# Kernel optimization log

Measured on AMD Instinct MI355X. Metric: run time of the kernel, lower is better.

## Reference

```python
import jax, jax.numpy as jnp
import numpy as np

N = 50000   # num nodes
D = 128     # dim_h = d_model = d_inner (expand=1)
E = 500000  # num edges
B, L = 4, 4096
K = 4       # d_conv
DS = 16     # d_state
DTR = 8     # dt_rank = ceil(128/16)


def setup_inputs() -> dict:
    key = jax.random.key(0)
    ks = jax.random.split(key, 32)
    rn = lambda i, shape, s=0.05: jax.random.normal(ks[i], shape, jnp.float32) * s
    inp = {}
    inp["graph_embeddings"] = jax.random.normal(ks[0], (N, D), jnp.float32)
    inp["graph_edges"] = jax.random.randint(ks[1], (2, E), 0, N)
    # unique node indices so the final scatter matches torch advanced indexing
    inp["sequence"] = jax.random.permutation(ks[2], N)[: B * L].reshape(B, L)
    # GatedGCN linears A,B,D,E (dim_h -> dim_h)
    inp["WA"] = rn(3, (D, D)); inp["bA"] = jnp.zeros((D,), jnp.float32)
    inp["WB"] = rn(4, (D, D)); inp["bB"] = jnp.zeros((D,), jnp.float32)
    inp["WD"] = rn(5, (D, D)); inp["bD"] = jnp.zeros((D,), jnp.float32)
    inp["WE"] = rn(6, (D, D)); inp["bE"] = jnp.zeros((D,), jnp.float32)
    # Mamba params
    inp["W_in"] = rn(7, (D, 2 * D))                 # in_proj (bias=False)
    inp["conv_w"] = rn(8, (D, 1, K))                # depthwise causal conv
    inp["conv_b"] = jnp.zeros((D,), jnp.float32)
    inp["W_x"] = rn(9, (D, DTR + 2 * DS))           # x_proj (bias=False)
    inp["W_dt"] = rn(10, (DTR, D))
    inp["b_dt"] = jnp.zeros((D,), jnp.float32)
    A_init = jnp.tile(jnp.arange(1, DS + 1, dtype=jnp.float32)[None, :], (D, 1))
    inp["A_log"] = jnp.log(A_init)
    inp["D_ssm"] = jnp.ones((D,), jnp.float32)
    inp["W_out"] = rn(11, (D, D))                   # out_proj (bias=False)
    # FFN
    inp["W1"] = rn(12, (D, 2 * D)); inp["b1"] = jnp.zeros((2 * D,), jnp.float32)
    inp["W2"] = rn(13, (2 * D, D)); inp["b2"] = jnp.zeros((D,), jnp.float32)
    return inp


def _gatedgcn(x, edges, WA, bA, WB, bB, WD, bD, WE, bE):
    src, dst = edges[0], edges[1]
    Ax = x @ WA + bA
    Bx = x @ WB + bB
    Dx = x @ WD + bD
    Ex = x @ WE + bE
    sigma = jax.nn.sigmoid(Dx[dst] + Ex[src])          # [E, D] edge gates
    num = jax.ops.segment_sum(sigma * Bx[src], dst, num_segments=N)
    den = jax.ops.segment_sum(sigma, dst, num_segments=N)
    out = Ax + num / (den + 1e-6)
    return x + jax.nn.relu(out)                        # residual (dropout=0, eval)


def _mamba(x, W_in, conv_w, conv_b, W_x, W_dt, b_dt, A_log, D_ssm, W_out):
    # x: [B, L, D]
    xz = x @ W_in
    xm, z = jnp.split(xz, 2, axis=-1)
    xc = jnp.transpose(xm, (0, 2, 1))                  # [B, D, L]
    xc = jax.lax.conv_general_dilated(
        xc, conv_w, (1,), [(K - 1, 0)],
        dimension_numbers=("NCH", "OIH", "NCH"), feature_group_count=D)
    xc = xc + conv_b[None, :, None]
    xm = jax.nn.silu(jnp.transpose(xc, (0, 2, 1)))     # [B, L, D]
    x_dbl = xm @ W_x
    dt, Bm, Cm = jnp.split(x_dbl, [DTR, DTR + DS], axis=-1)
    delta = jax.nn.softplus(dt @ W_dt + b_dt)          # [B, L, D]
    A = -jnp.exp(A_log)                                # [D, DS]
    dA = jnp.exp(delta[..., None] * A)                 # [B, L, D, DS]
    dBx = delta[..., None] * Bm[:, :, None, :] * xm[..., None]

    def step(h, t):
        dA_t, dBx_t, C_t = t
        h = dA_t * h + dBx_t                           # [B, D, DS]
        y = jnp.einsum("bdn,bn->bd", h, C_t)
        return h, y

    h0 = jnp.zeros((x.shape[0], D, DS), xm.dtype)
    _, ys = jax.lax.scan(step, h0, (jnp.swapaxes(dA, 0, 1),
                                    jnp.swapaxes(dBx, 0, 1),
                                    jnp.swapaxes(Cm, 0, 1)))
    y = jnp.swapaxes(ys, 0, 1) + xm * D_ssm
    y = y * jax.nn.silu(z)
    return y @ W_out


def reference(graph_embeddings, WA, bA, WB, bB, WD, bD, WE, bE,
              W_in, conv_w, conv_b, W_x, W_dt, b_dt, A_log, D_ssm, W_out,
              W1, b1, W2, b2, graph_edges, sequence):
    h_in1 = graph_embeddings[sequence]                 # [B, L, D]
    h_local = _gatedgcn(graph_embeddings, graph_edges, WA, bA, WB, bB, WD, bD, WE, bE)
    h1 = h_local[sequence]
    h_attn = h_in1 + _mamba(h_in1, W_in, conv_w, conv_b, W_x, W_dt, b_dt, A_log, D_ssm, W_out)
    h = h1 + h_attn
    h = h + (jax.nn.relu(h @ W1 + b1) @ W2 + b2)       # residual FFN
    flat = sequence.reshape(-1)
    emb = graph_embeddings.at[flat].set(
        0.5 * graph_embeddings[flat] + 0.5 * h.reshape(-1, D))
    return emb
```

## Files before the change

kernel.cpp:

```cpp
#include <hip/hip_runtime.h>
#include <hip/hip_bf16.h>

#define N_NODES 50000
#define DIM     128
#define NEDGE   500000
#define BB      4
#define LL      4096
#define NTOK    (BB*LL)
#define DSTATE  16
#define DTRANK  8
#define SCH     16
#define NCH     (LL/SCH)
#define NBDN    (BB*DIM*DSTATE)

typedef __attribute__((ext_vector_type(8))) short short8;
typedef __attribute__((ext_vector_type(4))) float f32x4;

static __device__ __forceinline__ float sigmoidf_(float x){ return 1.f/(1.f+__expf(-x)); }
static __device__ __forceinline__ float siluf_(float x){ return x/(1.f+__expf(-x)); }
static __device__ __forceinline__ float softplusf_(float x){ return (x > 20.f) ? x : log1pf(__expf(x)); }
static __device__ __forceinline__ short f2bf(float f){
  union { float f; unsigned u; } v; v.f = f;
  unsigned r = v.u + 0x7FFFu + ((v.u >> 16) & 1u);
  return (short)(r >> 16);
}
static __device__ __forceinline__ unsigned cvt2bf(float a, float b){
  unsigned r;
  asm("v_cvt_pk_bf16_f32 %0, %1, %2" : "=v"(r) : "v"(a), "v"(b));
  return r;
}
static __device__ __forceinline__ float bf2f(unsigned short u){
  union { unsigned u; float f; } v; v.u = ((unsigned)u) << 16; return v.f;
}

__global__ void prep_k(const float* __restrict__ x, const int* __restrict__ seq,
                       const float* __restrict__ WA, const float* __restrict__ WB,
                       const float* __restrict__ WD, const float* __restrict__ WE,
                       const float* __restrict__ W_in, const float* __restrict__ Wout,
                       const float* __restrict__ W1, const float* __restrict__ W2,
                       const float* __restrict__ W_x,
                       short* __restrict__ wpak, short* __restrict__ xbf,
                       short* __restrict__ hseqbf, int* __restrict__ invmap,
                       int* __restrict__ cnt){
  int blk = blockIdx.x, tid = threadIdx.x;
  if (blk < 736){
    int i = blk*256 + tid;
    float v;
    if (i < 32768){ int n=i>>7, k=i&127; v = (n<128)? WB[k*128+n] : WE[k*128+n-128]; }
    else if (i < 65536){ int j=i-32768, n=j>>7, k=j&127; v = (n<128)? WA[k*128+n] : WD[k*128+n-128]; }
    else if (i < 98304){ int j=i-65536, n=j>>7, k=j&127; v = W_in[k*256+n]; }
    else if (i < 131072){ int j=i-98304, n=j>>7, k=j&127; v = W1[k*256+n]; }
    else if (i < 163840){ int j=i-131072, n=j>>8, k=j&255; v = W2[k*128+n]; }
    else if (i < 180224){ int j=i-163840, n=j>>7, k=j&127; v = Wout[k*128+n]; }
    else if (i < 188416){ int j=i-180224, n=j>>7, k=j&127; v = (n<40)? W_x[k*40+n] : 0.f; }
    else return;
    wpak[i] = f2bf(v);
  } else if (blk < 3861){
    int i = (blk-736)*256 + tid;
    const float4 v0 = *(const float4*)(x + (size_t)i*8);
    const float4 v1 = *(const float4*)(x + (size_t)i*8 + 4);
    union { int4 q; short8 s; } w;
    w.q.x = cvt2bf(v0.x, v0.y); w.q.y = cvt2bf(v0.z, v0.w);
    w.q.z = cvt2bf(v1.x, v1.y); w.q.w = cvt2bf(v1.z, v1.w);
    *(short8*)(xbf + (size_t)i*8) = w.s;
  } else if (blk < 4885){
    int i = (blk-3861)*256 + tid;
    int t = i >> 4, cc = i & 15;
    const float* src = x + (size_t)seq[t]*128 + cc*8;
    const float4 v0 = *(const float4*)src;
    const float4 v1 = *(const float4*)(src + 4);
    union { int4 q; short8 s; } w;
    w.q.x = cvt2bf(v0.x, v0.y); w.q.y = cvt2bf(v0.z, v0.w);
    w.q.z = cvt2bf(v1.x, v1.y); w.q.w = cvt2bf(v1.z, v1.w);
    *(short8*)(hseqbf + (size_t)t*128 + cc*8) = w.s;
  } else if (blk < 4949){
    int i = (blk-4885)*256 + tid;
    if (i < NTOK) invmap[seq[i]] = i;
  } else {
    int i = (blk-4949)*256 + tid;
    if (i < 16384) cnt[i] = 0;
  }
}

template<int NCG, int KF, int EPI>
__global__ __launch_bounds__(256) void gemm4_k(const short* __restrict__ A,
    const short* __restrict__ Wt, const float* __restrict__ bias,
    float* __restrict__ C, short* __restrict__ C16, int ldc, int nsteps){
  const int K = KF*32;
  const int tid = threadIdx.x;
  const int wave = tid >> 6, lane = tid & 63;
  const int lr = lane & 15, kg = lane >> 4;
  const int cg = wave % NCG, rg = wave / NCG;
  const int RPB = 16*(4/NCG);

  short8 wf[4][KF];
  #pragma unroll
  for (int f=0; f<4; ++f){
    const short* wp = Wt + (size_t)(cg*64 + f*16 + lr)*K + kg*8;
    #pragma unroll
    for (int ks=0; ks<KF; ++ks) wf[f][ks] = *(const short8*)(wp + ks*32);
  }
  float4 bfv[4];
  #pragma unroll
  for (int f=0; f<4; ++f)
    bfv[f] = bias ? *(const float4*)&bias[cg*64 + f*16 + kg*4] : make_float4(0,0,0,0);

  int step = blockIdx.x;
  short8 a0[KF], a1[KF];
  if (step < nsteps){
    const short* p = A + ((size_t)step*RPB + rg*16 + lr)*K + kg*8;
    #pragma unroll
    for (int ks=0; ks<KF; ++ks) a0[ks] = *(const short8*)(p + ks*32);
  }
  for (; step < nsteps; step += gridDim.x){
    int nstep = step + gridDim.x;
    if (nstep < nsteps){
      const short* p = A + ((size_t)nstep*RPB + rg*16 + lr)*K + kg*8;
      #pragma unroll
      for (int ks=0; ks<KF; ++ks) a1[ks] = *(const short8*)(p + ks*32);
    }
    f32x4 acc[4];
    #pragma unroll
    for (int f=0; f<4; ++f) acc[f] = (f32x4){0.f,0.f,0.f,0.f};
    #pragma unroll
    for (int f=0; f<4; ++f)
      #pragma unroll
      for (int ks=0; ks<KF; ++ks)
        acc[f] = __builtin_amdgcn_mfma_f32_16x16x32_bf16(wf[f][ks], a0[ks], acc[f], 0,0,0);

    int row = step*RPB + rg*16 + lr;
    #pragma unroll
    for (int f=0; f<4; ++f){
      int col = cg*64 + f*16 + kg*4;
      size_t idx = (size_t)row*ldc + col;
      float v0 = acc[f][0]+bfv[f].x, v1 = acc[f][1]+bfv[f].y;
      float v2 = acc[f][2]+bfv[f].z, v3 = acc[f][3]+bfv[f].w;
      if (EPI == 0){
        *(float4*)&C[idx] = make_float4(v0,v1,v2,v3);
      } else if (EPI == 2){
        float4 c = *(const float4*)&C[idx];
        *(float4*)&C[idx] = make_float4(c.x+v0, c.y+v1, c.z+v2, c.w+v3);
      } else if (EPI == 3){
        uint2 u; u.x = cvt2bf(v0,v1); u.y = cvt2bf(v2,v3);
        *(uint2*)&C16[idx] = u;
      } else if (EPI == 4){
        float4 c = *(const float4*)&C[idx];
        float n0=c.x+v0, n1=c.y+v1, n2=c.z+v2, n3=c.w+v3;
        *(float4*)&C[idx] = make_float4(n0,n1,n2,n3);
        uint2 u; u.x = cvt2bf(n0,n1); u.y = cvt2bf(n2,n3);
        *(uint2*)&C16[idx] = u;
      } else {
        uint2 u; u.x = cvt2bf(fmaxf(v0,0.f), fmaxf(v1,0.f));
        u.y = cvt2bf(fmaxf(v2,0.f), fmaxf(v3,0.f));
        *(uint2*)&C16[idx] = u;
      }
    }
    #pragma unroll
    for (int ks=0; ks<KF; ++ks) a0[ks] = a1[ks];
  }
}

__global__ void edge_cnt_k(const int* __restrict__ ge, const int* __restrict__ invmap,
                           int* __restrict__ cnt){
  int e = blockIdx.x*256 + threadIdx.x;
  if (e >= NEDGE) return;
  int r = invmap[ge[NEDGE + e]];
  if (r >= 0) atomicAdd(&cnt[r], 1);
}

__global__ __launch_bounds__(1024) void rowptr_k(int* __restrict__ cnt, int* __restrict__ rowptr){
  __shared__ int part[1024];
  int t = threadIdx.x;
  int local[16];
  int s = 0;
  #pragma unroll
  for (int i=0;i<16;i++){ local[i] = s; s += cnt[t*16+i]; }
  part[t] = s;
  __syncthreads();
  for (int d=1; d<1024; d<<=1){
    int v = (t>=d) ? part[t-d] : 0;
    __syncthreads();
    part[t] += v;
    __syncthreads();
  }
  int base = (t==0) ? 0 : part[t-1];
  #pragma unroll
  for (int i=0;i<16;i++){ rowptr[t*16+i] = base + local[i]; cnt[t*16+i] = 0; }
  if (t == 1023) rowptr[16384] = part[1023];
}

__global__ void edge_scat_k(const int* __restrict__ ge, const int* __restrict__ invmap,
                            const int* __restrict__ rowptr, int* __restrict__ cnt,
                            int* __restrict__ esrc){
  int e = blockIdx.x*256 + threadIdx.x;
  if (e >= NEDGE) return;
  int r = invmap[ge[NEDGE + e]];
  if (r >= 0){
    int slot = rowptr[r] + atomicAdd(&cnt[r], 1);
    esrc[slot] = ge[e];
  }
}

__global__ __launch_bounds__(128) void agg_k(const int* __restrict__ rowptr,
    const int* __restrict__ esrc, const unsigned short* __restrict__ ADbf,
    const unsigned short* __restrict__ BE16, const unsigned short* __restrict__ hseqbf,
    float* __restrict__ hacc){
  int r = blockIdx.x, d = threadIdx.x;
  int e0 = rowptr[r], e1 = rowptr[r+1];
  float Dv = bf2f(ADbf[(size_t)r*256 + 128 + d]);
  float num = 0.f, den = 0.f;
  int s = (e0 < e1) ? esrc[e0] : 0;
  for (int i = e0; i < e1; ++i){
    int sn = (i+1 < e1) ? esrc[i+1] : 0;
    float bv = bf2f(BE16[(size_t)s*256 + d]);
    float ev = bf2f(BE16[(size_t)s*256 + 128 + d]);
    float sig = sigmoidf_(Dv + ev);
    num = fmaf(sig, bv, num);
    den += sig;
    s = sn;
  }
  float q = num / (den + 1e-6f);
  hacc[(size_t)r*DIM + d] = 2.f*bf2f(hseqbf[(size_t)r*DIM + d])
                          + fmaxf(bf2f(ADbf[(size_t)r*256 + d]) + q, 0.f);
}

__global__ void conv_silu_k(const unsigned short* __restrict__ xz, const float* __restrict__ cw,
                            const float* __restrict__ cb, short* __restrict__ xms){
  int row = blockIdx.x, d = threadIdx.x;
  int l = row & (LL-1);
  float acc = cb[d];
  #pragma unroll
  for (int k = 0; k < 4; ++k){
    int lo = l + k - 3;
    if (lo >= 0) acc = fmaf(cw[d*4+k], bf2f(xz[(size_t)(row + k - 3)*256 + d]), acc);
  }
  xms[(size_t)row*DIM + d] = f2bf(siluf_(acc));
}

__global__ __launch_bounds__(256) void scanA_k(const unsigned short* __restrict__ xms,
    const float* __restrict__ xdbl64, const float* __restrict__ Wdt,
    const float* __restrict__ bdt, const float* __restrict__ A_log,
    float* __restrict__ chP, float* __restrict__ chS){
  __shared__ float xd[2][SCH][64];
  int half = threadIdx.x >> 7, d = threadIdx.x & 127;
  int ch = blockIdx.x*2 + half;
  int b = ch >> 8, c = ch & (NCH-1);
  int r0 = b*LL + c*SCH;
  for (int i = d; i < SCH*16; i += 128){
    int row = i >> 4, c4 = i & 15;
    *(float4*)&xd[half][row][c4*4] = *(const float4*)&xdbl64[((size_t)(r0+row))*64 + c4*4];
  }
  __syncthreads();
  float wdt[8];
  #pragma unroll
  for (int k=0;k<8;k++) wdt[k] = Wdt[k*DIM + d];
  float bd = bdt[d];
  float An[16];
  {
    const float4* ap = (const float4*)&A_log[d*16];
    #pragma unroll
    for (int q=0;q<4;q++){
      float4 v = ap[q];
      An[q*4+0] = -__expf(v.x); An[q*4+1] = -__expf(v.y);
      An[q*4+2] = -__expf(v.z); An[q*4+3] = -__expf(v.w);
    }
  }
  float P[16], S[16];
  #pragma unroll
  for (int n=0;n<16;n++){ P[n]=1.f; S[n]=0.f; }
  for (int li=0; li<SCH; ++li){
    const float* xr = &xd[half][li][0];
    float xv = bf2f(xms[(size_t)(r0+li)*DIM + d]);
    float dt = bd;
    #pragma unroll
    for (int k=0;k<8;k++) dt = fmaf(xr[k], wdt[k], dt);
    float dl = softplusf_(dt);
    float t = dl * xv;
    #pragma unroll
    for (int n=0;n<16;n++){
      float a = __expf(dl*An[n]);
      S[n] = fmaf(a, S[n], t*xr[8+n]);
      P[n] *= a;
    }
  }
  size_t base = ((size_t)(c*BB + b)*DIM + d)*16;
  float4* pP = (float4*)&chP[base];
  float4* pS = (float4*)&chS[base];
  #pragma unroll
  for (int q=0;q<4;q++){
    pP[q] = make_float4(P[q*4],P[q*4+1],P[q*4+2],P[q*4+3]);
    pS[q] = make_float4(S[q*4],S[q*4+1],S[q*4+2],S[q*4+3]);
  }
}

__global__ void scanB_k(const float* __restrict__ chP, const float* __restrict__ chS,
                        float* __restrict__ chH){
  int bdn = blockIdx.x*256 + threadIdx.x;
  float carry = 0.f;
  #pragma unroll 4
  for (int c=0;c<NCH;++c){
    size_t idx = (size_t)c*NBDN + bdn;
    chH[idx] = carry;
    carry = fmaf(chP[idx], carry, chS[idx]);
  }
}

__global__ __launch_bounds__(256) void scanC_k(const unsigned short* __restrict__ xms,
    const float* __restrict__ xdbl64, const float* __restrict__ Wdt,
    const float* __restrict__ bdt, const float* __restrict__ A_log,
    const float* __restrict__ chH, const unsigned short* __restrict__ xz,
    const float* __restrict__ Dssm, short* __restrict__ y){
  __shared__ float xd[2][SCH][64];
  int half = threadIdx.x >> 7, d = threadIdx.x & 127;
  int ch = blockIdx.x*2 + half;
  int b = ch >> 8, c = ch & (NCH-1);
  int r0 = b*LL + c*SCH;
  for (int i = d; i < SCH*16; i += 128){
    int row = i >> 4, c4 = i & 15;
    *(float4*)&xd[half][row][c4*4] = *(const float4*)&xdbl64[((size_t)(r0+row))*64 + c4*4];
  }
  __syncthreads();
  float wdt[8];
  #pragma unroll
  for (int k=0;k<8;k++) wdt[k] = Wdt[k*DIM + d];
  float bd = bdt[d];
  float Dd = Dssm[d];
  float An[16];
  {
    const float4* ap = (const float4*)&A_log[d*16];
    #pragma unroll
    for (int q=0;q<4;q++){
      float4 v = ap[q];
      An[q*4+0] = -__expf(v.x); An[q*4+1] = -__expf(v.y);
      An[q*4+2] = -__expf(v.z); An[q*4+3] = -__expf(v.w);
    }
  }
  float h[16];
  {
    const float4* hp = (const float4*)&chH[((size_t)(c*BB + b)*DIM + d)*16];
    #pragma unroll
    for (int q=0;q<4;q++){
      float4 v = hp[q];
      h[q*4+0]=v.x; h[q*4+1]=v.y; h[q*4+2]=v.z; h[q*4+3]=v.w;
    }
  }
  for (int li=0; li<SCH; ++li){
    const float* xr = &xd[half][li][0];
    size_t row = r0 + li;
    float xv = bf2f(xms[row*DIM + d]);
    float dt = bd;
    #pragma unroll
    for (int k=0;k<8;k++) dt = fmaf(xr[k], wdt[k], dt);
    float dl = softplusf_(dt);
    float t = dl * xv;
    float acc = 0.f;
    #pragma unroll
    for (int n=0;n<16;n++){
      float a = __expf(dl*An[n]);
      h[n] = fmaf(a, h[n], t*xr[8+n]);
      acc = fmaf(h[n], xr[24+n], acc);
    }
    float zv = bf2f(xz[row*256 + 128 + d]);
    y[row*DIM + d] = f2bf((acc + xv*Dd) * siluf_(zv));
  }
}

__global__ void final_k(const float4* __restrict__ x, const int* __restrict__ invmap,
                        const float4* __restrict__ hacc, float4* __restrict__ out){
  int gid = blockIdx.x*256 + threadIdx.x;
  int node = gid >> 5, d4 = gid & 31;
  float4 v = x[gid];
  int r = invmap[node];
  if (r >= 0){
    float4 hb = hacc[(size_t)r*32 + d4];
    v.x = 0.5f*(v.x + hb.x); v.y = 0.5f*(v.y + hb.y);
    v.z = 0.5f*(v.z + hb.z); v.w = 0.5f*(v.w + hb.w);
  }
  out[gid] = v;
}

extern "C" void kernel_launch(void* const* d_in, const int* in_sizes, int n_in,
                              void* d_out, int out_size, void* d_ws, size_t ws_size,
                              hipStream_t stream) {
  const float* x      = (const float*)d_in[0];
  const int*   ge     = (const int*)  d_in[1];
  const int*   seq    = (const int*)  d_in[2];
  const float* WA = (const float*)d_in[3];
  const float* WB = (const float*)d_in[5];
  const float* WD = (const float*)d_in[7];
  const float* WE = (const float*)d_in[9];
  const float* W_in  = (const float*)d_in[11];
  const float* convw = (const float*)d_in[12];
  const float* convb = (const float*)d_in[13];
  const float* W_x   = (const float*)d_in[14];
  const float* W_dt  = (const float*)d_in[15];
  const float* b_dt  = (const float*)d_in[16];
  const float* A_log = (const float*)d_in[17];
  const float* D_ssm = (const float*)d_in[18];
  const float* W_out = (const float*)d_in[19];
  const float* W1 = (const float*)d_in[20]; const float* b1 = (const float*)d_in[21];
  const float* W2 = (const float*)d_in[22]; const float* b2 = (const float*)d_in[23];
  float* out = (float*)d_out;

  const size_t T = (size_t)NTOK*DIM;
  int* invmap = (int*)d_ws;
  int* cnt    = invmap + 50048;
  int* rowptr = cnt + 16384;
  int* esrc   = rowptr + 16400;
  short* wpak = (short*)(esrc + 500224);
  short* xbf    = wpak + 188416 + 32;
  short* hseqbf = xbf + (size_t)N_NODES*DIM;
  short* BE16   = hseqbf + T;
  short* xzbf   = BE16 + (size_t)N_NODES*256;
  short* ADbf   = xzbf + (size_t)NTOK*256;
  short* xmsbf  = ADbf + (size_t)NTOK*256;
  float* hacc  = (float*)(xmsbf + T);
  float* xdbl64= hacc + T;
  float* chP   = xdbl64 + (size_t)NTOK*64;
  float* chS   = chP + (size_t)NCH*NBDN;
  float* chH   = chS + (size_t)NCH*NBDN;
  size_t need = (size_t)((char*)(chH + (size_t)NCH*NBDN) - (char*)d_ws);
  if (ws_size < need) return;
  short* ybf    = xbf;
  short* haccbf = hseqbf;
  short* ffntbf = xzbf;

  const short* Wbe_t  = wpak;
  const short* Wad_t  = wpak + 32768;
  const short* Win_t  = wpak + 65536;
  const short* W1_t   = wpak + 98304;
  const short* W2_t   = wpak + 131072;
  const short* Wout_t = wpak + 163840;
  const short* Wxp_t  = wpak + 180224;

  hipMemsetAsync(invmap, 0xFF, (size_t)50048*4, stream);
  prep_k<<<5013, 256, 0, stream>>>(x, seq, WA, WB, WD, WE, W_in, W_out, W1, W2, W_x,
                                   wpak, xbf, hseqbf, invmap, cnt);

  gemm4_k<4,4,3><<<1024, 256, 0, stream>>>(xbf,    Wbe_t, nullptr, nullptr, BE16, 256, 3125);
  gemm4_k<4,4,3><<<1024, 256, 0, stream>>>(hseqbf, Wad_t, nullptr, nullptr, ADbf, 256, 1024);

  edge_cnt_k<<<(NEDGE+255)/256, 256, 0, stream>>>(ge, invmap, cnt);
  rowptr_k<<<1, 1024, 0, stream>>>(cnt, rowptr);
  edge_scat_k<<<(NEDGE+255)/256, 256, 0, stream>>>(ge, invmap, rowptr, cnt, esrc);
  agg_k<<<NTOK, 128, 0, stream>>>(rowptr, esrc, (const unsigned short*)ADbf,
                                  (const unsigned short*)BE16,
                                  (const unsigned short*)hseqbf, hacc);

  gemm4_k<4,4,3><<<1024, 256, 0, stream>>>(hseqbf, Win_t, nullptr, nullptr, xzbf, 256, 1024);
  conv_silu_k<<<NTOK, 128, 0, stream>>>((const unsigned short*)xzbf, convw, convb, xmsbf);
  gemm4_k<1,4,0><<<256, 256, 0, stream>>>(xmsbf, Wxp_t, nullptr, xdbl64, nullptr, 64, 256);
  scanA_k<<<BB*NCH/2, 256, 0, stream>>>((const unsigned short*)xmsbf, xdbl64, W_dt, b_dt, A_log, chP, chS);
  scanB_k<<<NBDN/256, 256, 0, stream>>>(chP, chS, chH);
  scanC_k<<<BB*NCH/2, 256, 0, stream>>>((const unsigned short*)xmsbf, xdbl64, W_dt, b_dt, A_log, chH,
                                        (const unsigned short*)xzbf, D_ssm, ybf);
  gemm4_k<2,4,4><<<512, 256, 0, stream>>>(ybf, Wout_t, nullptr, hacc, haccbf, 128, 512);

  gemm4_k<4,4,5><<<1024, 256, 0, stream>>>(haccbf, W1_t, b1, nullptr, ffntbf, 256, 1024);
  gemm4_k<2,8,2><<<512, 256, 0, stream>>>(ffntbf, W2_t, b2, hacc, nullptr, 128, 512);

  final_k<<<(N_NODES*DIM/4)/256, 256, 0, stream>>>((const float4*)x, invmap, (const float4*)hacc, (float4*)out);
}
```

Baseline: 265.9 us.

## Fuse final scatter into FFN GEMM epilogue and merge three input GEMMs

Copies x to the output inside prep_k and writes the scattered 0.5*(x+h) rows directly from the W2 GEMM epilogue, removing the separate final_k pass over the full embedding table. Three independent GEMMs (BE, AD, in_proj) are merged into one launch to cut launch overhead and fill the GPU better. The invmap memset is dropped, and stale entries are instead validated by checking seq[r]==dst. This risks a race if the out copy and the scatter writes are not ordered, but they are in separate kernels, so they are ordered.

```diff
diff --git a/kernel.cpp b/kernel.cpp
--- a/kernel.cpp
+++ b/kernel.cpp
@@ -41,7 +41,7 @@
                        const float* __restrict__ W_x,
                        short* __restrict__ wpak, short* __restrict__ xbf,
                        short* __restrict__ hseqbf, int* __restrict__ invmap,
-                       int* __restrict__ cnt){
+                       int* __restrict__ cnt, float* __restrict__ outp){
   int blk = blockIdx.x, tid = threadIdx.x;
   if (blk < 736){
     int i = blk*256 + tid;
@@ -59,6 +59,8 @@
     int i = (blk-736)*256 + tid;
     const float4 v0 = *(const float4*)(x + (size_t)i*8);
     const float4 v1 = *(const float4*)(x + (size_t)i*8 + 4);
+    *(float4*)(outp + (size_t)i*8)     = v0;
+    *(float4*)(outp + (size_t)i*8 + 4) = v1;
     union { int4 q; short8 s; } w;
     w.q.x = cvt2bf(v0.x, v0.y); w.q.y = cvt2bf(v0.z, v0.w);
     w.q.z = cvt2bf(v1.x, v1.y); w.q.w = cvt2bf(v1.z, v1.w);
@@ -83,9 +85,11 @@
 }
 
 template<int NCG, int KF, int EPI>
-__global__ __launch_bounds__(256) void gemm4_k(const short* __restrict__ A,
+static __device__ __forceinline__ void gemm4_body(const short* __restrict__ A,
     const short* __restrict__ Wt, const float* __restrict__ bias,
-    float* __restrict__ C, short* __restrict__ C16, int ldc, int nsteps){
+    float* __restrict__ C, short* __restrict__ C16, int ldc, int nsteps,
+    int bid, int nblk,
+    const int* __restrict__ seqp, const float* __restrict__ xg, float* __restrict__ outp){
   const int K = KF*32;
   const int tid = threadIdx.x;
   const int wave = tid >> 6, lane = tid & 63;
@@ -105,15 +109,15 @@
   for (int f=0; f<4; ++f)
     bfv[f] = bias ? *(const float4*)&bias[cg*64 + f*16 + kg*4] : make_float4(0,0,0,0);
 
-  int step = blockIdx.x;
+  int step = bid;
   short8 a0[KF], a1[KF];
   if (step < nsteps){
     const short* p = A + ((size_t)step*RPB + rg*16 + lr)*K + kg*8;
     #pragma unroll
     for (int ks=0; ks<KF; ++ks) a0[ks] = *(const short8*)(p + ks*32);
   }
-  for (; step < nsteps; step += gridDim.x){
-    int nstep = step + gridDim.x;
+  for (; step < nsteps; step += nblk){
+    int nstep = step + nblk;
     if (nstep < nsteps){
       const short* p = A + ((size_t)nstep*RPB + rg*16 + lr)*K + kg*8;
       #pragma unroll
@@ -149,10 +153,18 @@
         *(float4*)&C[idx] = make_float4(n0,n1,n2,n3);
         uint2 u; u.x = cvt2bf(n0,n1); u.y = cvt2bf(n2,n3);
         *(uint2*)&C16[idx] = u;
-      } else {
+      } else if (EPI == 5){
         uint2 u; u.x = cvt2bf(fmaxf(v0,0.f), fmaxf(v1,0.f));
         u.y = cvt2bf(fmaxf(v2,0.f), fmaxf(v3,0.f));
         *(uint2*)&C16[idx] = u;
+      } else {
+        float4 c = *(const float4*)&C[idx];
+        float n0=c.x+v0, n1=c.y+v1, n2=c.z+v2, n3=c.w+v3;
+        int sr = seqp[row];
+        const float4 xv = *(const float4*)(xg + (size_t)sr*128 + col);
+        float4 o = make_float4(0.5f*(xv.x+n0), 0.5f*(xv.y+n1),
+                               0.5f*(xv.z+n2), 0.5f*(xv.w+n3));
+        *(float4*)(outp + (size_t)sr*128 + col) = o;
       }
     }
     #pragma unroll
@@ -160,12 +172,34 @@
   }
 }
 
+template<int NCG, int KF, int EPI>
+__global__ __launch_bounds__(256) void gemm4_k(const short* __restrict__ A,
+    const short* __restrict__ Wt, const float* __restrict__ bias,
+    float* __restrict__ C, short* __restrict__ C16, int ldc, int nsteps,
+    const int* __restrict__ seqp, const float* __restrict__ xg, float* __restrict__ outp){
+  gemm4_body<NCG,KF,EPI>(A, Wt, bias, C, C16, ldc, nsteps, blockIdx.x, gridDim.x, seqp, xg, outp);
+}
+
+__global__ __launch_bounds__(256) void gemm3x_k(
+    const short* __restrict__ A0, const short* __restrict__ W0t, short* __restrict__ C0, int ns0,
+    const short* __restrict__ A1, const short* __restrict__ W1t, short* __restrict__ C1, int ns1,
+    const short* __restrict__ A2, const short* __restrict__ W2t, short* __restrict__ C2, int ns2){
+  int job = blockIdx.x >> 10, bid = blockIdx.x & 1023;
+  if (job == 0)
+    gemm4_body<4,4,3>(A0, W0t, nullptr, nullptr, C0, 256, ns0, bid, 1024, nullptr, nullptr, nullptr);
+  else if (job == 1)
+    gemm4_body<4,4,3>(A1, W1t, nullptr, nullptr, C1, 256, ns1, bid, 1024, nullptr, nullptr, nullptr);
+  else
+    gemm4_body<4,4,3>(A2, W2t, nullptr, nullptr, C2, 256, ns2, bid, 1024, nullptr, nullptr, nullptr);
+}
+
 __global__ void edge_cnt_k(const int* __restrict__ ge, const int* __restrict__ invmap,
-                           int* __restrict__ cnt){
+                           const int* __restrict__ seq, int* __restrict__ cnt){
   int e = blockIdx.x*256 + threadIdx.x;
   if (e >= NEDGE) return;
-  int r = invmap[ge[NEDGE + e]];
-  if (r >= 0) atomicAdd(&cnt[r], 1);
+  int dst = ge[NEDGE + e];
+  int r = invmap[dst];
+  if ((unsigned)r < NTOK && seq[r] == dst) atomicAdd(&cnt[r], 1);
 }
 
 __global__ __launch_bounds__(1024) void rowptr_k(int* __restrict__ cnt, int* __restrict__ rowptr){
@@ -190,12 +224,14 @@
 }
 
 __global__ void edge_scat_k(const int* __restrict__ ge, const int* __restrict__ invmap,
+                            const int* __restrict__ seq,
                             const int* __restrict__ rowptr, int* __restrict__ cnt,
                             int* __restrict__ esrc){
   int e = blockIdx.x*256 + threadIdx.x;
   if (e >= NEDGE) return;
-  int r = invmap[ge[NEDGE + e]];
-  if (r >= 0){
+  int dst = ge[NEDGE + e];
+  int r = invmap[dst];
+  if ((unsigned)r < NTOK && seq[r] == dst){
     int slot = rowptr[r] + atomicAdd(&cnt[r], 1);
     esrc[slot] = ge[e];
   }
@@ -363,20 +399,6 @@
     float zv = bf2f(xz[row*256 + 128 + d]);
     y[row*DIM + d] = f2bf((acc + xv*Dd) * siluf_(zv));
   }
-}
-
-__global__ void final_k(const float4* __restrict__ x, const int* __restrict__ invmap,
-                        const float4* __restrict__ hacc, float4* __restrict__ out){
-  int gid = blockIdx.x*256 + threadIdx.x;
-  int node = gid >> 5, d4 = gid & 31;
-  float4 v = x[gid];
-  int r = invmap[node];
-  if (r >= 0){
-    float4 hb = hacc[(size_t)r*32 + d4];
-    v.x = 0.5f*(v.x + hb.x); v.y = 0.5f*(v.y + hb.y);
-    v.z = 0.5f*(v.z + hb.z); v.w = 0.5f*(v.w + hb.w);
-  }
-  out[gid] = v;
 }
 
 extern "C" void kernel_launch(void* const* d_in, const int* in_sizes, int n_in,
@@ -433,31 +455,32 @@
   const short* Wout_t = wpak + 163840;
   const short* Wxp_t  = wpak + 180224;
 
-  hipMemsetAsync(invmap, 0xFF, (size_t)50048*4, stream);
   prep_k<<<5013, 256, 0, stream>>>(x, seq, WA, WB, WD, WE, W_in, W_out, W1, W2, W_x,
-                                   wpak, xbf, hseqbf, invmap, cnt);
-
-  gemm4_k<4,4,3><<<1024, 256, 0, stream>>>(xbf,    Wbe_t, nullptr, nullptr, BE16, 256, 3125);
-  gemm4_k<4,4,3><<<1024, 256, 0, stream>>>(hseqbf, Wad_t, nullptr, nullptr, ADbf, 256, 1024);
-
-  edge_cnt_k<<<(NEDGE+255)/256, 256, 0, stream>>>(ge, invmap, cnt);
+                                   wpak, xbf, hseqbf, invmap, cnt, out);
+
+  gemm3x_k<<<3072, 256, 0, stream>>>(xbf, Wbe_t, BE16, 3125,
+                                     hseqbf, Wad_t, ADbf, 1024,
+                                     hseqbf, Win_t, xzbf, 1024);
+
+  edge_cnt_k<<<(NEDGE+255)/256, 256, 0, stream>>>(ge, invmap, seq, cnt);
   rowptr_k<<<1, 1024, 0, stream>>>(cnt, rowptr);
-  edge_scat_k<<<(NEDGE+255)/256, 256, 0, stream>>>(ge, invmap, rowptr, cnt, esrc);
+  edge_scat_k<<<(NEDGE+255)/256, 256, 0, stream>>>(ge, invmap, seq, rowptr, cnt, esrc);
   agg_k<<<NTOK, 128, 0, stream>>>(rowptr, esrc, (const unsigned short*)ADbf,
                                   (const unsigned short*)BE16,
                                   (const unsigned short*)hseqbf, hacc);
 
-  gemm4_k<4,4,3><<<1024, 256, 0, stream>>>(hseqbf, Win_t, nullptr, nullptr, xzbf, 256, 1024);
   conv_silu_k<<<NTOK, 128, 0, stream>>>((const unsigned short*)xzbf, convw, convb, xmsbf);
-  gemm4_k<1,4,0><<<256, 256, 0, stream>>>(xmsbf, Wxp_t, nullptr, xdbl64, nullptr, 64, 256);
+  gemm4_k<1,4,0><<<256, 256, 0, stream>>>(xmsbf, Wxp_t, nullptr, xdbl64, nullptr, 64, 256,
+                                          nullptr, nullptr, nullptr);
   scanA_k<<<BB*NCH/2, 256, 0, stream>>>((const unsigned short*)xmsbf, xdbl64, W_dt, b_dt, A_log, chP, chS);
   scanB_k<<<NBDN/256, 256, 0, stream>>>(chP, chS, chH);
   scanC_k<<<BB*NCH/2, 256, 0, stream>>>((const unsigned short*)xmsbf, xdbl64, W_dt, b_dt, A_log, chH,
                                         (const unsigned short*)xzbf, D_ssm, ybf);
-  gemm4_k<2,4,4><<<512, 256, 0, stream>>>(ybf, Wout_t, nullptr, hacc, haccbf, 128, 512);
-
-  gemm4_k<4,4,5><<<1024, 256, 0, stream>>>(haccbf, W1_t, b1, nullptr, ffntbf, 256, 1024);
-  gemm4_k<2,8,2><<<512, 256, 0, stream>>>(ffntbf, W2_t, b2, hacc, nullptr, 128, 512);
-
-  final_k<<<(N_NODES*DIM/4)/256, 256, 0, stream>>>((const float4*)x, invmap, (const float4*)hacc, (float4*)out);
-}
+  gemm4_k<2,4,4><<<512, 256, 0, stream>>>(ybf, Wout_t, nullptr, hacc, haccbf, 128, 512,
+                                          nullptr, nullptr, nullptr);
+
+  gemm4_k<4,4,5><<<1024, 256, 0, stream>>>(haccbf, W1_t, b1, nullptr, ffntbf, 256, 1024,
+                                           nullptr, nullptr, nullptr);
+  gemm4_k<2,8,6><<<512, 256, 0, stream>>>(ffntbf, W2_t, b2, hacc, nullptr, 128, 512,
+                                          seq, x, out);
+}
```

New measurement: 252.0 us. -5.2%, faster.
